# Kernel optimization log

Hardware: AMD Instinct MI355X
Metric: run time of the kernel (lower is better)

The kernel has to match this reference:

```python
import jax, jax.numpy as jnp
import numpy as np

N_NODES, D_IN, D_OUT = 1_000_000, 128, 128
M_PATHS, N_INST, PATH_LEN, N_ETYPES = 6, 20_000, 4, 6


def setup_inputs() -> dict:
    key = jax.random.key(0)
    ks = jax.random.split(key, 9)
    scale = 1.0 / np.sqrt(D_IN)
    features = jax.random.normal(ks[0], (N_NODES, D_IN), jnp.float32)
    instances = jax.random.randint(ks[1], (M_PATHS, N_INST, PATH_LEN), 0, N_NODES, dtype=jnp.int64)
    edge_types = jax.random.randint(ks[2], (M_PATHS,), 0, N_ETYPES, dtype=jnp.int64)
    W_enc = jax.random.normal(ks[3], (M_PATHS, D_IN, D_OUT), jnp.float32) * scale
    b_enc = jax.random.normal(ks[4], (M_PATHS, D_OUT), jnp.float32) * scale
    W_att = jax.random.normal(ks[5], (N_ETYPES, 2 * D_OUT), jnp.float32) * scale
    b_att = jax.random.normal(ks[6], (N_ETYPES,), jnp.float32) * scale
    w_mp = jax.random.normal(ks[7], (D_OUT,), jnp.float32) * scale
    b_mp = jax.random.normal(ks[8], (), jnp.float32) * scale
    return {"features": features, "W_enc": W_enc, "b_enc": b_enc, "W_att": W_att,
            "b_att": b_att, "w_mp": w_mp, "b_mp": b_mp,
            "instances": instances, "edge_types": edge_types}


def reference(features, W_enc, b_enc, W_att, b_att, w_mp, b_mp, instances, edge_types):
    # Gather node features for every metapath instance: [M, I, L, D]
    gathered = features[instances]
    # Per-metapath linear encoder: [M, I, L, H]
    encoded = jnp.einsum('mild,mdh->milh', gathered, W_enc) + b_enc[:, None, None, :]
    first = encoded[:, :, 0, :]   # [M, I, H]
    last = encoded[:, :, -1, :]   # [M, I, H]
    cat = jnp.concatenate([first, last], axis=-1)  # [M, I, 2H]
    # Edge-type-specific attention (Linear(2H, 1)) selected per metapath
    Wsel = W_att[edge_types]      # [M, 2H]
    bsel = b_att[edge_types]      # [M]
    scores = jnp.einsum('mik,mk->mi', cat, Wsel) + bsel[:, None]  # [M, I]
    w = jax.nn.softmax(jax.nn.leaky_relu(scores, 0.2), axis=1)    # softmax over instances
    mp_out = jnp.einsum('mi,mih->mh', w, last)                    # [M, H]
    # Metapath-level attention
    mp_scores = mp_out @ w_mp + b_mp                              # [M]
    mw = jax.nn.softmax(jax.nn.leaky_relu(mp_scores, 0.2), axis=0)
    out = jnp.sum(mw[:, None] * mp_out, axis=0)                   # [H]
    return jax.nn.elu(out)
```

## Files before the change

### kernel.cpp

```cpp
#include <hip/hip_runtime.h>
#include <hip/hip_bf16.h>
#include <math.h>

#define NPATH 6
#define NINST 20000
#define PLEN 4
#define DFEAT 128
#define TPB1 256
#define WPB 4
#define GPW 4
#define GPB (WPB * GPW)
#define BPP 128
#define GPP (BPP * GPB)

__device__ __forceinline__ float dot4(float4 a, float4 b) {
    return a.x * b.x + a.y * b.y + a.z * b.z + a.w * b.w;
}

__global__ __launch_bounds__(TPB1, 4) void k_pass1(
    const float* __restrict__ feat, const int* __restrict__ inst,
    const float* __restrict__ W_enc, const float* __restrict__ b_enc,
    const float* __restrict__ W_att, const float* __restrict__ b_att,
    const int* __restrict__ etype,
    float* __restrict__ pV, float* __restrict__ pM, float* __restrict__ pS)
{
    int m    = blockIdx.x / BPP;
    int bw   = blockIdx.x % BPP;
    int tid  = threadIdx.x;
    int wv   = tid >> 6, lane = tid & 63;
    int grp  = lane >> 4, sub = lane & 15;
    int gid  = wv * GPW + grp;
    int g    = bw * GPB + gid;

    __shared__ float swa[2 * DFEAT];
    __shared__ float su1[DFEAT], su2[DFEAT];
    __shared__ float sbc[DFEAT];
    __shared__ float scv;
    __shared__ float sV[GPB][DFEAT + 4];
    __shared__ float sMx[GPB], sSm[GPB];

    const int4* ib4 = (const int4*)(inst + (size_t)m * NINST * PLEN);
    int i = g;
    int4 ja = ib4[i];
    const float4* r0 = (const float4*)(feat + (size_t)ja.x * DFEAT);
    const float4* r3 = (const float4*)(feat + (size_t)ja.w * DFEAT);
    float4 f0a = r0[sub], f0b = r0[sub + 16];
    float4 f3a = r3[sub], f3b = r3[sub + 16];
    int4 jb = ib4[i + GPP];

    int e = etype[m];
    swa[tid] = W_att[(size_t)e * (2 * DFEAT) + tid];
    __syncthreads();
    if (tid < DFEAT) {
        const float4* Wr = (const float4*)(W_enc + ((size_t)m * DFEAT + tid) * DFEAT);
        float s1 = 0.f, s2 = 0.f;
        #pragma unroll 8
        for (int q = 0; q < DFEAT / 4; ++q) {
            float4 w4 = Wr[q];
            s1 += w4.x * swa[4*q]         + w4.y * swa[4*q+1]
                + w4.z * swa[4*q+2]       + w4.w * swa[4*q+3];
            s2 += w4.x * swa[DFEAT+4*q]   + w4.y * swa[DFEAT+4*q+1]
                + w4.z * swa[DFEAT+4*q+2] + w4.w * swa[DFEAT+4*q+3];
        }
        su1[tid] = s1;
        su2[tid] = s2;
        sbc[tid] = b_enc[m * DFEAT + tid] * (swa[tid] + swa[DFEAT + tid]);
    }
    __syncthreads();
    if (tid < 64) {
        float t = sbc[tid] + sbc[tid + 64];
        #pragma unroll
        for (int o = 32; o; o >>= 1) t += __shfl_xor(t, o);
        if (tid == 0) scv = t + b_att[e];
    }
    __syncthreads();

    float4 U1a = ((const float4*)su1)[sub], U1b = ((const float4*)su1)[sub + 16];
    float4 U2a = ((const float4*)su2)[sub], U2b = ((const float4*)su2)[sub + 16];
    float c = scv;

    float mx = -3e38f, sum = 0.f;
    float4 va = make_float4(0.f, 0.f, 0.f, 0.f);
    float4 vb = make_float4(0.f, 0.f, 0.f, 0.f);

    while (i < NINST) {
        int inx = i + GPP, ipf = i + 2 * GPP;
        int4 jc = jb;
        if (ipf < NINST) jc = ib4[ipf];
        float4 g0a = f0a, g0b = f0b, g3a = f3a, g3b = f3b;
        if (inx < NINST) {
            const float4* q0 = (const float4*)(feat + (size_t)jb.x * DFEAT);
            const float4* q3 = (const float4*)(feat + (size_t)jb.w * DFEAT);
            g0a = q0[sub]; g0b = q0[sub + 16];
            g3a = q3[sub]; g3b = q3[sub + 16];
        }

        float p = dot4(f0a, U1a) + dot4(f0b, U1b) + dot4(f3a, U2a) + dot4(f3b, U2b);
        p += __shfl_xor(p, 1);
        p += __shfl_xor(p, 2);
        p += __shfl_xor(p, 4);
        p += __shfl_xor(p, 8);
        float s = p + c;
        s = s > 0.f ? s : 0.2f * s;
        float ns    = fmaxf(mx, s);
        float scale = __expf(mx - ns);
        float pe    = __expf(s - ns);
        sum = sum * scale + pe;
        va.x = va.x * scale + pe * f3a.x;  va.y = va.y * scale + pe * f3a.y;
        va.z = va.z * scale + pe * f3a.z;  va.w = va.w * scale + pe * f3a.w;
        vb.x = vb.x * scale + pe * f3b.x;  vb.y = vb.y * scale + pe * f3b.y;
        vb.z = vb.z * scale + pe * f3b.z;  vb.w = vb.w * scale + pe * f3b.w;
        mx = ns;

        f0a = g0a; f0b = g0b; f3a = g3a; f3b = g3b;
        jb = jc;
        i = inx;
    }

    *(float4*)&sV[gid][sub * 4]      = va;
    *(float4*)&sV[gid][64 + sub * 4] = vb;
    if (sub == 0) { sMx[gid] = mx; sSm[gid] = sum; }
    __syncthreads();

    if (tid < DFEAT) {
        float M = sMx[0];
        #pragma unroll
        for (int k = 1; k < GPB; ++k) M = fmaxf(M, sMx[k]);
        float S = 0.f, V = 0.f;
        #pragma unroll
        for (int k = 0; k < GPB; ++k) {
            float ek = __expf(sMx[k] - M);
            S += ek * sSm[k];
            V += ek * sV[k][tid];
        }
        pV[(size_t)blockIdx.x * DFEAT + tid] = V;
        if (tid == 0) { pM[blockIdx.x] = M; pS[blockIdx.x] = S; }
    }
}

__global__ __launch_bounds__(256) void k_pass2(
    const float* __restrict__ pV, const float* __restrict__ pM, const float* __restrict__ pS,
    const float* __restrict__ W_enc, const float* __restrict__ b_enc,
    const float* __restrict__ w_mp, const float* __restrict__ b_mp,
    float* __restrict__ mp_out, float* __restrict__ ms)
{
    int m = blockIdx.x, tid = threadIdx.x;
    int d = tid & 127, slice = tid >> 7;

    __shared__ float tmp[BPP];
    __shared__ float eL[BPP];
    __shared__ float sv[2][DFEAT];
    __shared__ float sVn[DFEAT];
    __shared__ float smp[DFEAT];
    __shared__ float sS, sMx;

    if (tid < BPP) tmp[tid] = pM[m * BPP + tid];
    __syncthreads();
    for (int off = 64; off; off >>= 1) {
        if (tid < off) tmp[tid] = fmaxf(tmp[tid], tmp[tid + off]);
        __syncthreads();
    }
    if (tid == 0) sMx = tmp[0];
    __syncthreads();
    float M = sMx;

    if (tid < BPP) {
        float ek = __expf(pM[m * BPP + tid] - M);
        eL[tid] = ek;
        tmp[tid] = ek * pS[m * BPP + tid];
    }
    __syncthreads();
    for (int off = 64; off; off >>= 1) {
        if (tid < off) tmp[tid] += tmp[tid + off];
        __syncthreads();
    }
    if (tid == 0) sS = tmp[0];
    __syncthreads();
    float Sinv = 1.f / sS;

    float acc = 0.f;
    for (int k = slice; k < BPP; k += 2)
        acc += eL[k] * pV[((size_t)(m * BPP + k)) * DFEAT + d];
    sv[slice][d] = acc;
    __syncthreads();
    if (tid < DFEAT) sVn[tid] = (sv[0][tid] + sv[1][tid]) * Sinv;
    __syncthreads();

    const float* W = W_enc + (size_t)m * DFEAT * DFEAT;
    float gacc = 0.f;
    for (int dd = slice; dd < DFEAT; dd += 2)
        gacc += sVn[dd] * W[(size_t)dd * DFEAT + d];
    __syncthreads();
    sv[slice][d] = gacc;
    __syncthreads();
    if (tid < DFEAT) {
        float t = sv[0][tid] + sv[1][tid] + b_enc[m * DFEAT + tid];
        mp_out[m * DFEAT + tid] = t;
        smp[tid] = t * w_mp[tid];
    }
    __syncthreads();

    if (tid < 64) {
        float t = smp[tid] + smp[tid + 64];
        #pragma unroll
        for (int o = 32; o; o >>= 1) t += __shfl_xor(t, o);
        if (tid == 0) ms[m] = t + b_mp[0];
    }
}

__global__ void k_final(const float* __restrict__ mp_out, const float* __restrict__ ms,
                        float* __restrict__ out) {
    int h = threadIdx.x;
    float l[NPATH], mx = -3e38f;
    #pragma unroll
    for (int m = 0; m < NPATH; ++m) {
        float x = ms[m];
        x = x > 0.f ? x : 0.2f * x;
        l[m] = x;
        mx = fmaxf(mx, x);
    }
    float sum = 0.f;
    #pragma unroll
    for (int m = 0; m < NPATH; ++m) { l[m] = __expf(l[m] - mx); sum += l[m]; }
    float o = 0.f;
    #pragma unroll
    for (int m = 0; m < NPATH; ++m) o += (l[m] / sum) * mp_out[m * DFEAT + h];
    out[h] = o > 0.f ? o : __expf(o) - 1.f;
}

extern "C" void kernel_launch(void* const* d_in, const int* in_sizes, int n_in,
                              void* d_out, int out_size, void* d_ws, size_t ws_size,
                              hipStream_t stream) {
    const float* features   = (const float*)d_in[0];
    const float* W_enc      = (const float*)d_in[1];
    const float* b_enc      = (const float*)d_in[2];
    const float* W_att      = (const float*)d_in[3];
    const float* b_att      = (const float*)d_in[4];
    const float* w_mp       = (const float*)d_in[5];
    const float* b_mp       = (const float*)d_in[6];
    const int*   instances  = (const int*)d_in[7];
    const int*   edge_types = (const int*)d_in[8];
    float* out = (float*)d_out;
    float* ws  = (float*)d_ws;

    const int nblk1 = NPATH * BPP;

    float* pV     = ws;
    float* pM     = pV + (size_t)nblk1 * DFEAT;
    float* pS     = pM + nblk1;
    float* mp_out = pS + nblk1;
    float* msv    = mp_out + NPATH * DFEAT;

    k_pass1<<<nblk1, TPB1, 0, stream>>>(features, instances, W_enc, b_enc,
                                        W_att, b_att, edge_types, pV, pM, pS);

    k_pass2<<<NPATH, 256, 0, stream>>>(pV, pM, pS, W_enc, b_enc, w_mp, b_mp, mp_out, msv);

    k_final<<<1, DFEAT, 0, stream>>>(mp_out, msv, out);
}
```

Before: 65.94 us.

## Deepen gather prefetch to two rows ahead and use lazy softmax rescaling

```diff
diff --git a/kernel.cpp b/kernel.cpp
--- a/kernel.cpp
+++ b/kernel.cpp
@@ -12,6 +12,7 @@
 #define GPB (WPB * GPW)
 #define BPP 128
 #define GPP (BPP * GPB)
+#define RESCALE_THR 8.0f
 
 __device__ __forceinline__ float dot4(float4 a, float4 b) {
     return a.x * b.x + a.y * b.y + a.z * b.z + a.w * b.w;
@@ -41,12 +42,18 @@
 
     const int4* ib4 = (const int4*)(inst + (size_t)m * NINST * PLEN);
     int i = g;
-    int4 ja = ib4[i];
-    const float4* r0 = (const float4*)(feat + (size_t)ja.x * DFEAT);
-    const float4* r3 = (const float4*)(feat + (size_t)ja.w * DFEAT);
-    float4 f0a = r0[sub], f0b = r0[sub + 16];
-    float4 f3a = r3[sub], f3b = r3[sub + 16];
-    int4 jb = ib4[i + GPP];
+    int4 j0 = ib4[i];
+    int4 j1 = ib4[i + GPP];
+    int4 j2 = ib4[i + 2 * GPP];
+
+    const float4* r0 = (const float4*)(feat + (size_t)j0.x * DFEAT);
+    const float4* r3 = (const float4*)(feat + (size_t)j0.w * DFEAT);
+    float4 A0a = r0[sub], A0b = r0[sub + 16];
+    float4 A3a = r3[sub], A3b = r3[sub + 16];
+    const float4* q0 = (const float4*)(feat + (size_t)j1.x * DFEAT);
+    const float4* q3 = (const float4*)(feat + (size_t)j1.w * DFEAT);
+    float4 B0a = q0[sub], B0b = q0[sub + 16];
+    float4 B3a = q3[sub], B3b = q3[sub + 16];
 
     int e = etype[m];
     swa[tid] = W_att[(size_t)e * (2 * DFEAT) + tid];
@@ -79,47 +86,62 @@
     float4 U2a = ((const float4*)su2)[sub], U2b = ((const float4*)su2)[sub + 16];
     float c = scv;
 
-    float mx = -3e38f, sum = 0.f;
+    float mref = 0.f, tmax = -3e38f, sum = 0.f;
     float4 va = make_float4(0.f, 0.f, 0.f, 0.f);
     float4 vb = make_float4(0.f, 0.f, 0.f, 0.f);
 
-    while (i < NINST) {
-        int inx = i + GPP, ipf = i + 2 * GPP;
-        int4 jc = jb;
-        if (ipf < NINST) jc = ib4[ipf];
-        float4 g0a = f0a, g0b = f0b, g3a = f3a, g3b = f3b;
-        if (inx < NINST) {
-            const float4* q0 = (const float4*)(feat + (size_t)jb.x * DFEAT);
-            const float4* q3 = (const float4*)(feat + (size_t)jb.w * DFEAT);
-            g0a = q0[sub]; g0b = q0[sub + 16];
-            g3a = q3[sub]; g3b = q3[sub + 16];
-        }
-
-        float p = dot4(f0a, U1a) + dot4(f0b, U1b) + dot4(f3a, U2a) + dot4(f3b, U2b);
-        p += __shfl_xor(p, 1);
-        p += __shfl_xor(p, 2);
-        p += __shfl_xor(p, 4);
-        p += __shfl_xor(p, 8);
-        float s = p + c;
-        s = s > 0.f ? s : 0.2f * s;
-        float ns    = fmaxf(mx, s);
-        float scale = __expf(mx - ns);
-        float pe    = __expf(s - ns);
-        sum = sum * scale + pe;
-        va.x = va.x * scale + pe * f3a.x;  va.y = va.y * scale + pe * f3a.y;
-        va.z = va.z * scale + pe * f3a.z;  va.w = va.w * scale + pe * f3a.w;
-        vb.x = vb.x * scale + pe * f3b.x;  vb.y = vb.y * scale + pe * f3b.y;
-        vb.z = vb.z * scale + pe * f3b.z;  vb.w = vb.w * scale + pe * f3b.w;
-        mx = ns;
-
-        f0a = g0a; f0b = g0b; f3a = g3a; f3b = g3b;
-        jb = jc;
-        i = inx;
-    }
+#define COMPUTE(R0a, R0b, R3a, R3b)                                          \
+    {                                                                        \
+        float p = dot4(R0a, U1a) + dot4(R0b, U1b)                            \
+                + dot4(R3a, U2a) + dot4(R3b, U2b);                           \
+        p += __shfl_xor(p, 1);                                               \
+        p += __shfl_xor(p, 2);                                               \
+        p += __shfl_xor(p, 4);                                               \
+        p += __shfl_xor(p, 8);                                               \
+        float s = p + c;                                                     \
+        s = s > 0.f ? s : 0.2f * s;                                          \
+        tmax = fmaxf(tmax, s);                                               \
+        if (tmax > mref + RESCALE_THR) {                                     \
+            float r = __expf(mref - tmax);                                   \
+            sum *= r;                                                        \
+            va.x *= r; va.y *= r; va.z *= r; va.w *= r;                      \
+            vb.x *= r; vb.y *= r; vb.z *= r; vb.w *= r;                      \
+            mref = tmax;                                                     \
+        }                                                                    \
+        float pe = __expf(s - mref);                                         \
+        sum += pe;                                                           \
+        va.x += pe * R3a.x; va.y += pe * R3a.y;                              \
+        va.z += pe * R3a.z; va.w += pe * R3a.w;                              \
+        vb.x += pe * R3b.x; vb.y += pe * R3b.y;                              \
+        vb.z += pe * R3b.z; vb.w += pe * R3b.w;                              \
+    }
+
+    while (i + 2 * GPP < NINST) {
+        const float4* p0 = (const float4*)(feat + (size_t)j2.x * DFEAT);
+        const float4* p3 = (const float4*)(feat + (size_t)j2.w * DFEAT);
+        float4 C0a = p0[sub], C0b = p0[sub + 16];
+        float4 C3a = p3[sub], C3b = p3[sub + 16];
+        int nj = i + 3 * GPP;
+        nj = nj < NINST ? nj : NINST - 1;
+        int4 j3 = ib4[nj];
+
+        COMPUTE(A0a, A0b, A3a, A3b);
+
+        A0a = B0a; A0b = B0b; A3a = B3a; A3b = B3b;
+        B0a = C0a; B0b = C0b; B3a = C3a; B3b = C3b;
+        j2 = j3;
+        i += GPP;
+    }
+
+    COMPUTE(A0a, A0b, A3a, A3b);
+    i += GPP;
+    if (i < NINST) COMPUTE(B0a, B0b, B3a, B3b);
+
+#undef COMPUTE
 
     *(float4*)&sV[gid][sub * 4]      = va;
     *(float4*)&sV[gid][64 + sub * 4] = vb;
-    if (sub == 0) { sMx[gid] = mx; sSm[gid] = sum; }
+    if (sub == 0) { sMx[gid] = mref; sSm[gid] = sum; }
     __syncthreads();
 
     if (tid < DFEAT) {
```

Result: no change. 65.83 us (median of 2 runs) (-0.2%).
